# Performance work log

Hardware: AMD Instinct MI355X
Metric: run time of the kernel (lower is better)

Reference implementation:

```python
import jax, jax.numpy as jnp
import numpy as np

B, S, H = 64, 512, 768
A1, C1 = 100, 300          # token-attention and sentence-classifier hidden sizes
BETA = 1.0                 # soft_attention_beta
SLW, TLW, RLW = 1.0, 1.0, 0.01  # loss weights


def setup_inputs() -> dict:
    key = jax.random.key(0)
    ks = jax.random.split(key, 12)
    hidden_states = jax.random.normal(ks[0], (B, S, H), jnp.float32)
    # token_attention: Linear(H,100) -> Tanh -> Linear(100,1) -> Sigmoid
    w1 = jax.random.normal(ks[1], (H, A1), jnp.float32) * 0.02
    b1 = jnp.zeros((A1,), jnp.float32)
    w2 = jax.random.normal(ks[2], (A1, 1), jnp.float32) * 0.02
    b2 = jnp.zeros((1,), jnp.float32)
    # sentence_classification: Linear(H,300) -> Tanh -> Linear(300,1) -> Sigmoid
    sw1 = jax.random.normal(ks[3], (H, C1), jnp.float32) * 0.02
    sb1 = jnp.zeros((C1,), jnp.float32)
    sw2 = jax.random.normal(ks[4], (C1, 1), jnp.float32) * 0.02
    sb2 = jnp.zeros((1,), jnp.float32)
    offset_mapping = jax.random.randint(ks[5], (B, S, 2), 0, 4).astype(jnp.int32)
    offset_mapping = offset_mapping.at[:, 0, 0].set(0)  # first token starts a word
    # labels in {-1, 0, 1}; -1 = ignore
    labels = jax.random.randint(ks[6], (B, S), -1, 2).astype(jnp.float32)
    return {
        "hidden_states": hidden_states,
        "w1": w1, "b1": b1, "w2": w2, "b2": b2,
        "sw1": sw1, "sb1": sb1, "sw2": sw2, "sb2": sb2,
        "labels": labels,
        "offset_mapping": offset_mapping,
    }


def _forward(hidden_states, w1, b1, w2, b2, sw1, sb1, sw2, sb2, labels, offset_mapping):
    # token attention scores in (0,1): [B, S]
    token_att = jax.nn.sigmoid(
        jnp.tanh(hidden_states @ w1 + b1) @ w2 + b2
    )[..., 0]

    # ragged per-word subword max-pooling (segment-max along the sequence)
    not_subword = offset_mapping[:, :, 0] == 0                 # [B, S] word starts
    seg = jnp.maximum(jnp.cumsum(not_subword.astype(jnp.int32), axis=1) - 1, 0)

    def _seg_max(vals, seg_ids):
        return jax.ops.segment_max(vals, seg_ids, num_segments=S)

    segmax = jax.vmap(_seg_max)(token_att, seg)                # [B, S] per-word max
    word_att = jnp.where(not_subword, jnp.take_along_axis(segmax, seg, axis=1), 0.0)

    # mask: labeled tokens that are word starts
    token_mask = ((labels != -1) & not_subword).astype(token_att.dtype)
    masked = word_att * token_mask                              # token_logits [B, S]

    # beta-normalized soft attention pooling over hidden states
    p = masked ** BETA
    att_norm = p / jnp.sum(p, axis=1, keepdims=True)            # [B, S]
    pooled = jnp.einsum("bsh,bs->bh", hidden_states, att_norm)  # [B, H]

    sent = jax.nn.sigmoid(jnp.tanh(pooled @ sw1 + sb1) @ sw2 + sb2)  # [B, 1]

    # losses (MSE with reduction='sum')
    sentence_labels = jnp.max(labels, axis=1, keepdims=True)    # [B, 1]
    sentence_loss = jnp.sum((sent - sentence_labels) ** 2)
    zero_labels = jnp.where(labels != -1, labels, 0.0)
    token_loss = jnp.sum((masked - zero_labels) ** 2)
    ones_masked = jnp.where(masked == 0, 1.0, masked)
    reg_a = jnp.sum(jnp.min(ones_masked, axis=1, keepdims=True) ** 2)
    reg_b = jnp.sum((jnp.max(masked, axis=1, keepdims=True) - sentence_labels) ** 2)
    total = SLW * sentence_loss + TLW * token_loss + RLW * (reg_a + reg_b)
    return total, sentence_loss, token_loss, reg_a, reg_b, masked, sent


def reference(hidden_states, w1, b1, w2, b2, sw1, sb1, sw2, sb2, labels, offset_mapping):
    return _forward(hidden_states, w1, b1, w2, b2, sw1, sb1, sw2, sb2,
                    labels, offset_mapping)
```

## Files before the change

kernel.cpp:

```cpp
#include <hip/hip_runtime.h>
#include <math.h>

#define BB 64
#define SS 512
#define HH 768
#define AA1 100
#define CC1 300

typedef __bf16 bf16x8 __attribute__((ext_vector_type(8)));
typedef float f32x4 __attribute__((ext_vector_type(4)));

#ifndef __has_builtin
#define __has_builtin(x) 0
#endif
#if __has_builtin(__builtin_amdgcn_global_load_lds)
#define HAVE_GLL 1
#else
#define HAVE_GLL 0
#endif

#define AS1 __attribute__((address_space(1)))
#define AS3 __attribute__((address_space(3)))

__global__ __launch_bounds__(256) void k_prep(const float* __restrict__ w1,
                                              __bf16* __restrict__ w1i) {
    int idx = blockIdx.x * 256 + threadIdx.x;
    int j = idx % 112;
    int r = idx / 112;
    int e = r & 7, g = r >> 3;
    int k = (g >> 2) * 32 + (g & 3) * 8 + e;
    float v = (j < AA1) ? w1[k * AA1 + j] : 0.f;
    w1i[((size_t)g * 112 + j) * 8 + e] = (__bf16)v;
}

__global__ __launch_bounds__(256) void k_token_att(
        const float* __restrict__ hs, const __bf16* __restrict__ w1i,
        const float* __restrict__ b1, const float* __restrict__ w2,
        const float* __restrict__ b2, float* __restrict__ token_att) {
    __shared__ __attribute__((aligned(16))) float lA[4096];
    __shared__ __attribute__((aligned(16))) __bf16 lB[3584];

    const int tid = threadIdx.x;
    const int tok0 = blockIdx.x * 128;
    const int w = tid >> 6, lane = tid & 63;
    const int q = lane >> 4, ln = lane & 15;
    const int t0 = w * 32 + ln;
    const int t1 = t0 + 16;

    f32x4 acc0[7], acc1[7];
#pragma unroll
    for (int n = 0; n < 7; n++) {
        acc0[n] = (f32x4){0.f, 0.f, 0.f, 0.f};
        acc1[n] = (f32x4){0.f, 0.f, 0.f, 0.f};
    }

    const int p0 = (2 * q) ^ (ln & 7);
    const int p1 = (2 * q + 1) ^ (ln & 7);

    for (int kt = 0; kt < 24; kt++) {
        const int ko = kt * 32;
#pragma unroll
        for (int it = 0; it < 4; it++) {
            int i = tid + it * 256;
            int tt = i >> 3, c = (i & 7) ^ (tt & 7);
            const float* g = hs + (size_t)(tok0 + tt) * HH + ko + c * 4;
#if HAVE_GLL
            __builtin_amdgcn_global_load_lds((AS1 void*)g,
                    (AS3 void*)(lA + (it * 256 + w * 64) * 4), 16, 0, 0);
#else
            *(f32x4*)&lA[i * 4] = *(const f32x4*)g;
#endif
        }
        {
            const __bf16* gb0 = w1i + (size_t)kt * 3584 + (size_t)tid * 8;
#if HAVE_GLL
            __builtin_amdgcn_global_load_lds((AS1 void*)gb0,
                    (AS3 void*)(lB + (w * 64) * 8), 16, 0, 0);
            if (w < 3) {
                const __bf16* gb1 = w1i + (size_t)kt * 3584 + (size_t)(tid + 256) * 8;
                __builtin_amdgcn_global_load_lds((AS1 void*)gb1,
                        (AS3 void*)(lB + (256 + w * 64) * 8), 16, 0, 0);
            }
#else
            *(bf16x8*)&lB[(size_t)tid * 8] = *(const bf16x8*)gb0;
            if (tid < 192) {
                const __bf16* gb1 = w1i + (size_t)kt * 3584 + (size_t)(tid + 256) * 8;
                *(bf16x8*)&lB[(size_t)(tid + 256) * 8] = *(const bf16x8*)gb1;
            }
#endif
        }
        __syncthreads();
        f32x4 a00 = *(f32x4*)&lA[(t0 * 8 + p0) * 4];
        f32x4 a01 = *(f32x4*)&lA[(t0 * 8 + p1) * 4];
        f32x4 a10 = *(f32x4*)&lA[(t1 * 8 + p0) * 4];
        f32x4 a11 = *(f32x4*)&lA[(t1 * 8 + p1) * 4];
        bf16x8 af0, af1;
#pragma unroll
        for (int e = 0; e < 4; e++) {
            af0[e] = (__bf16)a00[e]; af0[e + 4] = (__bf16)a01[e];
            af1[e] = (__bf16)a10[e]; af1[e + 4] = (__bf16)a11[e];
        }
#pragma unroll
        for (int n = 0; n < 7; n++) {
            bf16x8 bf = *(bf16x8*)&lB[((size_t)q * 112 + n * 16 + ln) * 8];
            acc0[n] = __builtin_amdgcn_mfma_f32_16x16x32_bf16(af0, bf, acc0[n], 0, 0, 0);
            acc1[n] = __builtin_amdgcn_mfma_f32_16x16x32_bf16(af1, bf, acc1[n], 0, 0, 0);
        }
        __syncthreads();
    }

    float s0 = 0.f, s1 = 0.f, s2 = 0.f, s3 = 0.f;
    float u0 = 0.f, u1 = 0.f, u2 = 0.f, u3 = 0.f;
#pragma unroll
    for (int n = 0; n < 7; n++) {
        int j = n * 16 + ln;
        if (j < AA1) {
            float bj = b1[j], wj = w2[j];
            s0 += tanhf(acc0[n][0] + bj) * wj;
            s1 += tanhf(acc0[n][1] + bj) * wj;
            s2 += tanhf(acc0[n][2] + bj) * wj;
            s3 += tanhf(acc0[n][3] + bj) * wj;
            u0 += tanhf(acc1[n][0] + bj) * wj;
            u1 += tanhf(acc1[n][1] + bj) * wj;
            u2 += tanhf(acc1[n][2] + bj) * wj;
            u3 += tanhf(acc1[n][3] + bj) * wj;
        }
    }
#pragma unroll
    for (int off = 1; off < 16; off <<= 1) {
        s0 += __shfl_xor(s0, off); s1 += __shfl_xor(s1, off);
        s2 += __shfl_xor(s2, off); s3 += __shfl_xor(s3, off);
        u0 += __shfl_xor(u0, off); u1 += __shfl_xor(u1, off);
        u2 += __shfl_xor(u2, off); u3 += __shfl_xor(u3, off);
    }
    if (ln == 0) {
        float bb = b2[0];
        int base0 = tok0 + w * 32 + q * 4;
        int base1 = base0 + 16;
        token_att[base0 + 0] = 1.f / (1.f + expf(-(s0 + bb)));
        token_att[base0 + 1] = 1.f / (1.f + expf(-(s1 + bb)));
        token_att[base0 + 2] = 1.f / (1.f + expf(-(s2 + bb)));
        token_att[base0 + 3] = 1.f / (1.f + expf(-(s3 + bb)));
        token_att[base1 + 0] = 1.f / (1.f + expf(-(u0 + bb)));
        token_att[base1 + 1] = 1.f / (1.f + expf(-(u1 + bb)));
        token_att[base1 + 2] = 1.f / (1.f + expf(-(u2 + bb)));
        token_att[base1 + 3] = 1.f / (1.f + expf(-(u3 + bb)));
    }
}

__global__ __launch_bounds__(512) void k_mask(
        const float* __restrict__ token_att, const float* __restrict__ labels,
        const int* __restrict__ offm, float* __restrict__ masked_out,
        float* __restrict__ cw_g, short* __restrict__ cs_g,
        int* __restrict__ nnz_g, float* __restrict__ inv_g,
        float4* __restrict__ stats_g) {
    __shared__ int smax[512];
    __shared__ int wscan[8];
    __shared__ int wscan2[8];
    __shared__ float wred[5][8];

    const int b = blockIdx.x, s = threadIdx.x;
    const int lane = s & 63, wv = s >> 6;
    const int ns = (offm[(b * SS + s) * 2] == 0) ? 1 : 0;

    int v = ns;
#pragma unroll
    for (int off = 1; off < 64; off <<= 1) {
        int o = __shfl_up(v, off);
        if (lane >= off) v += o;
    }
    if (lane == 63) wscan[wv] = v;
    smax[s] = 0;
    __syncthreads();
    int woff = 0;
    for (int i = 0; i < 8; i++) woff += (i < wv) ? wscan[i] : 0;
    const int seg = max(v + woff - 1, 0);

    const float ta = token_att[b * SS + s];
    atomicMax(&smax[seg], __float_as_int(ta));
    __syncthreads();

    const float wa = ns ? __int_as_float(smax[seg]) : 0.f;
    const float lab = labels[b * SS + s];
    const float m = (lab != -1.f && ns) ? wa : 0.f;
    masked_out[b * SS + s] = m;

    const float zl = (lab != -1.f) ? lab : 0.f;
    const float tl = (m - zl) * (m - zl);
    const float ones = (m == 0.f) ? 1.f : m;

    float r0 = m, r1 = tl, r2 = m, r3 = ones, r4 = lab;
#pragma unroll
    for (int off = 32; off > 0; off >>= 1) {
        r0 += __shfl_xor(r0, off);
        r1 += __shfl_xor(r1, off);
        r2 = fmaxf(r2, __shfl_xor(r2, off));
        r3 = fminf(r3, __shfl_xor(r3, off));
        r4 = fmaxf(r4, __shfl_xor(r4, off));
    }
    if (lane == 0) {
        wred[0][wv] = r0; wred[1][wv] = r1; wred[2][wv] = r2;
        wred[3][wv] = r3; wred[4][wv] = r4;
    }

    const int nz = (m != 0.f) ? 1 : 0;
    int v2 = nz;
#pragma unroll
    for (int off = 1; off < 64; off <<= 1) {
        int o = __shfl_up(v2, off);
        if (lane >= off) v2 += o;
    }
    if (lane == 63) wscan2[wv] = v2;
    __syncthreads();

    int woff2 = 0;
    for (int i = 0; i < 8; i++) woff2 += (i < wv) ? wscan2[i] : 0;
    if (nz) {
        int pos = v2 + woff2 - 1;
        cw_g[b * SS + pos] = m;
        cs_g[b * SS + pos] = (short)s;
    }
    if (s == 0) {
        float att = 0.f, tokl = 0.f, maxm = -1e30f, minone = 1e30f, slab = -1e30f;
        int nnz = 0;
        for (int i = 0; i < 8; i++) {
            att += wred[0][i]; tokl += wred[1][i];
            maxm = fmaxf(maxm, wred[2][i]);
            minone = fminf(minone, wred[3][i]);
            slab = fmaxf(slab, wred[4][i]);
            nnz += wscan2[i];
        }
        nnz_g[b] = nnz;
        inv_g[b] = 1.f / att;
        stats_g[b] = make_float4(tokl, maxm, minone, slab);
    }
}

__global__ __launch_bounds__(256) void k_pool(
        const float* __restrict__ hs, const float* __restrict__ cw_g,
        const short* __restrict__ cs_g, const int* __restrict__ nnz_g,
        const float* __restrict__ inv_g, float* __restrict__ pooled,
        float* __restrict__ zsum) {
    __shared__ float wl[SS];
    __shared__ short il[SS];
    __shared__ float red[256];

    const int b = blockIdx.x, hc = blockIdx.y;
    const int tid = threadIdx.x;
    const int nnz = nnz_g[b];
    if (hc == 0 && tid == 0) zsum[b] = 0.f;
    if (tid < nnz) { wl[tid] = cw_g[b * SS + tid]; il[tid] = cs_g[b * SS + tid]; }
    if (tid + 256 < nnz) {
        wl[tid + 256] = cw_g[b * SS + tid + 256];
        il[tid + 256] = cs_g[b * SS + tid + 256];
    }
    __syncthreads();

    const int h = (tid & 63) + hc * 64;
    const int slot = tid >> 6;
    const float* hsb = hs + (size_t)b * SS * HH + h;
    const int len = (nnz + 3) >> 2;
    const int i0 = slot * len;
    const int i1 = min(i0 + len, nnz);
    float a0 = 0.f, a1 = 0.f, a2 = 0.f, a3 = 0.f;
    int i = i0;
    for (; i + 4 <= i1; i += 4) {
        a0 += hsb[(size_t)il[i]     * HH] * wl[i];
        a1 += hsb[(size_t)il[i + 1] * HH] * wl[i + 1];
        a2 += hsb[(size_t)il[i + 2] * HH] * wl[i + 2];
        a3 += hsb[(size_t)il[i + 3] * HH] * wl[i + 3];
    }
    for (; i < i1; i++) a0 += hsb[(size_t)il[i] * HH] * wl[i];
    red[tid] = (a0 + a1) + (a2 + a3);
    __syncthreads();
    if (tid < 64)
        pooled[(size_t)b * HH + h] =
            (red[tid] + red[tid + 64] + red[tid + 128] + red[tid + 192]) * inv_g[b];
}

__global__ __launch_bounds__(256) void k_sent(
        const float* __restrict__ pooled, const float* __restrict__ sw1,
        const float* __restrict__ sb1, const float* __restrict__ sw2,
        float* __restrict__ zsum) {
    __shared__ float pl[HH];
    __shared__ float red[256];

    const int b = blockIdx.x, cc = blockIdx.y;
    const int tid = threadIdx.x;
    pl[tid]       = pooled[(size_t)b * HH + tid];
    pl[tid + 256] = pooled[(size_t)b * HH + tid + 256];
    pl[tid + 512] = pooled[(size_t)b * HH + tid + 512];
    __syncthreads();

    const int cl = tid & 63, kq = tid >> 6;
    const int c = cc * 60 + cl;
    float z = 0.f;
    if (cl < 60) {
        const int k0 = kq * 192;
        for (int k = k0; k < k0 + 192; k += 8) {
#pragma unroll
            for (int u = 0; u < 8; u++)
                z += pl[k + u] * sw1[(size_t)(k + u) * CC1 + c];
        }
    }
    red[tid] = z;
    __syncthreads();
    if (kq == 0) {
        float zz = red[tid] + red[tid + 64] + red[tid + 128] + red[tid + 192];
        float t = 0.f;
        if (cl < 60) t = tanhf(zz + sb1[c]) * sw2[c];
#pragma unroll
        for (int off = 32; off > 0; off >>= 1) t += __shfl_xor(t, off);
        if (cl == 0) atomicAdd(&zsum[b], t);
    }
}

__global__ __launch_bounds__(64) void k_losses(
        const float* __restrict__ zsum, const float* __restrict__ sb2,
        const float4* __restrict__ stats_g, float* __restrict__ sent_out,
        float* __restrict__ out) {
    const int b = threadIdx.x;
    const float sv = 1.f / (1.f + expf(-(zsum[b] + sb2[0])));
    sent_out[b] = sv;
    const float4 st = stats_g[b];
    float vs = sv - st.w; vs *= vs;
    float ra = st.z * st.z;
    float rb = st.y - st.w; rb *= rb;
    float s0 = vs, s1 = st.x, s2 = ra, s3 = rb;
#pragma unroll
    for (int off = 32; off > 0; off >>= 1) {
        s0 += __shfl_xor(s0, off);
        s1 += __shfl_xor(s1, off);
        s2 += __shfl_xor(s2, off);
        s3 += __shfl_xor(s3, off);
    }
    if (b == 0) {
        out[1] = s0; out[2] = s1; out[3] = s2; out[4] = s3;
        out[0] = s0 + s1 + 0.01f * (s2 + s3);
    }
}

extern "C" void kernel_launch(void* const* d_in, const int* in_sizes, int n_in,
                              void* d_out, int out_size, void* d_ws, size_t ws_size,
                              hipStream_t stream) {
    const float* hs  = (const float*)d_in[0];
    const float* w1  = (const float*)d_in[1];
    const float* b1  = (const float*)d_in[2];
    const float* w2  = (const float*)d_in[3];
    const float* b2  = (const float*)d_in[4];
    const float* sw1 = (const float*)d_in[5];
    const float* sb1 = (const float*)d_in[6];
    const float* sw2 = (const float*)d_in[7];
    const float* sb2 = (const float*)d_in[8];
    const float* labels = (const float*)d_in[9];
    const int*   offm   = (const int*)d_in[10];

    float* out = (float*)d_out;
    float* ws  = (float*)d_ws;

    float*  token_att = ws;
    __bf16* w1i    = (__bf16*)(ws + 32768);
    float*  cw     = ws + 32768 + 43008;
    short*  cs     = (short*)(cw + 32768);
    int*    nnz    = (int*)(cw + 32768 + 16384);
    float*  inv    = (float*)(nnz + 64);
    float4* stats  = (float4*)(inv + 64);
    float*  pooled = ws;
    float*  zsum   = ws + 49152;

    float* masked_out = out + 5;
    float* sent_out   = out + 5 + BB * SS;

    hipLaunchKernelGGL(k_prep, dim3(336), dim3(256), 0, stream, w1, w1i);
    hipLaunchKernelGGL(k_token_att, dim3(256), dim3(256), 0, stream,
                       hs, w1i, b1, w2, b2, token_att);
    hipLaunchKernelGGL(k_mask, dim3(BB), dim3(512), 0, stream,
                       token_att, labels, offm, masked_out,
                       cw, cs, nnz, inv, stats);
    hipLaunchKernelGGL(k_pool, dim3(BB, 12), dim3(256), 0, stream,
                       hs, cw, cs, nnz, inv, pooled, zsum);
    hipLaunchKernelGGL(k_sent, dim3(BB, 5), dim3(256), 0, stream,
                       pooled, sw1, sb1, sw2, zsum);
    hipLaunchKernelGGL(k_losses, dim3(1), dim3(64), 0, stream,
                       zsum, sb2, stats, sent_out, out);
}
```

Baseline: 211.6 us.

## Load token-attention MFMA operands directly from global memory, dropping LDS staging

The token-attention GEMM kernel no longer stages hidden-state and weight tiles through shared memory with barriers. Each lane now reads its MFMA operands straight from global memory, and each block handles 64 tokens instead of 128, so the grid doubles to 512 blocks for more parallelism and no __syncthreads. In exchange, global loads are less coalesced: each lane reads two 16-byte chunks per row. The weight operand is re-read from global or cache by every wave instead of being shared through LDS.

```diff
diff --git a/kernel.cpp b/kernel.cpp
--- a/kernel.cpp
+++ b/kernel.cpp
@@ -37,114 +37,61 @@
         const float* __restrict__ hs, const __bf16* __restrict__ w1i,
         const float* __restrict__ b1, const float* __restrict__ w2,
         const float* __restrict__ b2, float* __restrict__ token_att) {
-    __shared__ __attribute__((aligned(16))) float lA[4096];
-    __shared__ __attribute__((aligned(16))) __bf16 lB[3584];
-
     const int tid = threadIdx.x;
-    const int tok0 = blockIdx.x * 128;
+    const int tok0 = blockIdx.x * 64;
     const int w = tid >> 6, lane = tid & 63;
     const int q = lane >> 4, ln = lane & 15;
-    const int t0 = w * 32 + ln;
-    const int t1 = t0 + 16;
-
-    f32x4 acc0[7], acc1[7];
-#pragma unroll
-    for (int n = 0; n < 7; n++) {
-        acc0[n] = (f32x4){0.f, 0.f, 0.f, 0.f};
-        acc1[n] = (f32x4){0.f, 0.f, 0.f, 0.f};
-    }
-
-    const int p0 = (2 * q) ^ (ln & 7);
-    const int p1 = (2 * q + 1) ^ (ln & 7);
-
+    const int trow = tok0 + w * 16 + ln;
+
+    f32x4 acc[7];
+#pragma unroll
+    for (int n = 0; n < 7; n++) acc[n] = (f32x4){0.f, 0.f, 0.f, 0.f};
+
+    const float* ga = hs + (size_t)trow * HH + q * 8;
+    const __bf16* gb = w1i + (size_t)(q * 112 + ln) * 8;
+
+#pragma unroll 4
     for (int kt = 0; kt < 24; kt++) {
-        const int ko = kt * 32;
-#pragma unroll
-        for (int it = 0; it < 4; it++) {
-            int i = tid + it * 256;
-            int tt = i >> 3, c = (i & 7) ^ (tt & 7);
-            const float* g = hs + (size_t)(tok0 + tt) * HH + ko + c * 4;
-#if HAVE_GLL
-            __builtin_amdgcn_global_load_lds((AS1 void*)g,
-                    (AS3 void*)(lA + (it * 256 + w * 64) * 4), 16, 0, 0);
-#else
-            *(f32x4*)&lA[i * 4] = *(const f32x4*)g;
-#endif
-        }
-        {
-            const __bf16* gb0 = w1i + (size_t)kt * 3584 + (size_t)tid * 8;
-#if HAVE_GLL
-            __builtin_amdgcn_global_load_lds((AS1 void*)gb0,
-                    (AS3 void*)(lB + (w * 64) * 8), 16, 0, 0);
-            if (w < 3) {
-                const __bf16* gb1 = w1i + (size_t)kt * 3584 + (size_t)(tid + 256) * 8;
-                __builtin_amdgcn_global_load_lds((AS1 void*)gb1,
-                        (AS3 void*)(lB + (256 + w * 64) * 8), 16, 0, 0);
-            }
-#else
-            *(bf16x8*)&lB[(size_t)tid * 8] = *(const bf16x8*)gb0;
-            if (tid < 192) {
-                const __bf16* gb1 = w1i + (size_t)kt * 3584 + (size_t)(tid + 256) * 8;
-                *(bf16x8*)&lB[(size_t)(tid + 256) * 8] = *(const bf16x8*)gb1;
-            }
-#endif
-        }
-        __syncthreads();
-        f32x4 a00 = *(f32x4*)&lA[(t0 * 8 + p0) * 4];
-        f32x4 a01 = *(f32x4*)&lA[(t0 * 8 + p1) * 4];
-        f32x4 a10 = *(f32x4*)&lA[(t1 * 8 + p0) * 4];
-        f32x4 a11 = *(f32x4*)&lA[(t1 * 8 + p1) * 4];
-        bf16x8 af0, af1;
+        f32x4 a0 = *(const f32x4*)(ga + kt * 32);
+        f32x4 a1 = *(const f32x4*)(ga + kt * 32 + 4);
+        bf16x8 af;
 #pragma unroll
         for (int e = 0; e < 4; e++) {
-            af0[e] = (__bf16)a00[e]; af0[e + 4] = (__bf16)a01[e];
-            af1[e] = (__bf16)a10[e]; af1[e + 4] = (__bf16)a11[e];
-        }
+            af[e] = (__bf16)a0[e];
+            af[e + 4] = (__bf16)a1[e];
+        }
+        const __bf16* gbk = gb + (size_t)kt * 3584;
 #pragma unroll
         for (int n = 0; n < 7; n++) {
-            bf16x8 bf = *(bf16x8*)&lB[((size_t)q * 112 + n * 16 + ln) * 8];
-            acc0[n] = __builtin_amdgcn_mfma_f32_16x16x32_bf16(af0, bf, acc0[n], 0, 0, 0);
-            acc1[n] = __builtin_amdgcn_mfma_f32_16x16x32_bf16(af1, bf, acc1[n], 0, 0, 0);
-        }
-        __syncthreads();
+            bf16x8 bf = *(const bf16x8*)(gbk + n * 128);
+            acc[n] = __builtin_amdgcn_mfma_f32_16x16x32_bf16(af, bf, acc[n], 0, 0, 0);
+        }
     }
 
     float s0 = 0.f, s1 = 0.f, s2 = 0.f, s3 = 0.f;
-    float u0 = 0.f, u1 = 0.f, u2 = 0.f, u3 = 0.f;
 #pragma unroll
     for (int n = 0; n < 7; n++) {
         int j = n * 16 + ln;
         if (j < AA1) {
             float bj = b1[j], wj = w2[j];
-            s0 += tanhf(acc0[n][0] + bj) * wj;
-            s1 += tanhf(acc0[n][1] + bj) * wj;
-            s2 += tanhf(acc0[n][2] + bj) * wj;
-            s3 += tanhf(acc0[n][3] + bj) * wj;
-            u0 += tanhf(acc1[n][0] + bj) * wj;
-            u1 += tanhf(acc1[n][1] + bj) * wj;
-            u2 += tanhf(acc1[n][2] + bj) * wj;
-            u3 += tanhf(acc1[n][3] + bj) * wj;
+            s0 += tanhf(acc[n][0] + bj) * wj;
+            s1 += tanhf(acc[n][1] + bj) * wj;
+            s2 += tanhf(acc[n][2] + bj) * wj;
+            s3 += tanhf(acc[n][3] + bj) * wj;
         }
     }
 #pragma unroll
     for (int off = 1; off < 16; off <<= 1) {
         s0 += __shfl_xor(s0, off); s1 += __shfl_xor(s1, off);
         s2 += __shfl_xor(s2, off); s3 += __shfl_xor(s3, off);
-        u0 += __shfl_xor(u0, off); u1 += __shfl_xor(u1, off);
-        u2 += __shfl_xor(u2, off); u3 += __shfl_xor(u3, off);
     }
     if (ln == 0) {
         float bb = b2[0];
-        int base0 = tok0 + w * 32 + q * 4;
-        int base1 = base0 + 16;
-        token_att[base0 + 0] = 1.f / (1.f + expf(-(s0 + bb)));
-        token_att[base0 + 1] = 1.f / (1.f + expf(-(s1 + bb)));
-        token_att[base0 + 2] = 1.f / (1.f + expf(-(s2 + bb)));
-        token_att[base0 + 3] = 1.f / (1.f + expf(-(s3 + bb)));
-        token_att[base1 + 0] = 1.f / (1.f + expf(-(u0 + bb)));
-        token_att[base1 + 1] = 1.f / (1.f + expf(-(u1 + bb)));
-        token_att[base1 + 2] = 1.f / (1.f + expf(-(u2 + bb)));
-        token_att[base1 + 3] = 1.f / (1.f + expf(-(u3 + bb)));
+        int base = tok0 + w * 16 + q * 4;
+        token_att[base + 0] = 1.f / (1.f + expf(-(s0 + bb)));
+        token_att[base + 1] = 1.f / (1.f + expf(-(s1 + bb)));
+        token_att[base + 2] = 1.f / (1.f + expf(-(s2 + bb)));
+        token_att[base + 3] = 1.f / (1.f + expf(-(s3 + bb)));
     }
 }
 
@@ -372,7 +319,7 @@
     float* sent_out   = out + 5 + BB * SS;
 
     hipLaunchKernelGGL(k_prep, dim3(336), dim3(256), 0, stream, w1, w1i);
-    hipLaunchKernelGGL(k_token_att, dim3(256), dim3(256), 0, stream,
+    hipLaunchKernelGGL(k_token_att, dim3(512), dim3(256), 0, stream,
                        hs, w1i, b1, w2, b2, token_att);
     hipLaunchKernelGGL(k_mask, dim3(BB), dim3(512), 0, stream,
                        token_att, labels, offm, masked_out,
```

Measured after the change: 209.0 us. About the same (-1.2%).
